# Optimization experiments

Hardware: AMD Instinct MI355X
Metric: run time of the kernel (lower is better)

## Reference

```python
import jax, jax.numpy as jnp
import numpy as np

T, D_IN, H, D_OUT = 20, 4, 768, 1
B = 1024


def setup_inputs() -> dict:
    key = jax.random.key(0)
    ks = jax.random.split(key, 8)
    s = 1.0 / np.sqrt(H)
    return {
        "batch_price": jax.random.normal(ks[0], (B, T, D_IN), jnp.float32),
        "batch_event": jax.random.normal(ks[1], (B, T, H), jnp.float32),
        "W_ih": jax.random.uniform(ks[2], (T, 4 * H, D_IN), jnp.float32, -s, s),
        "W_hh": jax.random.uniform(ks[3], (T, 4 * H, H), jnp.float32, -s, s),
        "b_ih": jax.random.uniform(ks[4], (T, 4 * H), jnp.float32, -s, s),
        "b_hh": jax.random.uniform(ks[5], (T, 4 * H), jnp.float32, -s, s),
        "fc_w": jax.random.uniform(ks[6], (D_OUT, H), jnp.float32, -s, s),
        "fc_b": jax.random.uniform(ks[7], (D_OUT,), jnp.float32, -s, s),
    }


def _lstm_cell(x, h_mat, c, wih, whh, bih, bhh):
    # gates: [B, 4H] in PyTorch LSTMCell order (i, f, g, o)
    gates = x @ wih.T + bih + h_mat @ whh.T + bhh
    i, f, g, o = jnp.split(gates, 4, axis=-1)
    c_next = jax.nn.sigmoid(f) * c + jax.nn.sigmoid(i) * jnp.tanh(g)
    h_next = jax.nn.sigmoid(o) * jnp.tanh(c_next)
    return h_next, c_next


def reference(batch_price, batch_event, W_ih, W_hh, b_ih, b_hh, fc_w, fc_b):
    Bb, Tt, _ = batch_price.shape
    Hh = W_hh.shape[-1]
    # step 0: hx = batch_event[:, 0], cell state = zeros
    h, c = _lstm_cell(batch_price[:, 0], batch_event[:, 0],
                      jnp.zeros((Bb, Hh), batch_price.dtype),
                      W_ih[0], W_hh[0], b_ih[0], b_hh[0])

    def step(carry, inp):
        h, c = carry
        x, ev, wih, whh, bih, bhh = inp
        # faithful to source: hx = torch.sum(batch_event_t + h_prev) -> scalar
        hx = jnp.sum(ev + h)
        h_mat = jnp.broadcast_to(hx, (Bb, Hh))
        h2, c2 = _lstm_cell(x, h_mat, c, wih, whh, bih, bhh)
        return (h2, c2), None

    xs = (jnp.swapaxes(batch_price[:, 1:], 0, 1),  # [T-1, B, D_IN]
          jnp.swapaxes(batch_event[:, 1:], 0, 1),  # [T-1, B, H]
          W_ih[1:], W_hh[1:], b_ih[1:], b_hh[1:])
    (h, c), _ = jax.lax.scan(step, (h, c), xs)
    return h @ fc_w.T + fc_b  # [B, 1]
```

## Files before the change

kernel.cpp:

```cpp
#include <hip/hip_runtime.h>
#include <stdint.h>

#define Bsz 1024
#define Tn  20
#define Hn  768
#define G4n 3072

#define WS_SH    0
#define WS_SEV   32
#define WS_PART  64
#define WS_RS    1088
#define WS_BS    (1088 + Tn*G4n)
#define WS_C     (1088 + 2*Tn*G4n)

#define NB_GEMM   768
#define NB_BIAS   240
#define NB_SEV    1216
#define NB_A      (NB_GEMM + NB_BIAS + NB_SEV)
#define NB_ROWSUM 3648

typedef float  floatx4 __attribute__((ext_vector_type(4)));
typedef short  bfrag8  __attribute__((ext_vector_type(8)));

__device__ __forceinline__ float wave_reduce(float v){
#pragma unroll
    for (int o = 32; o > 0; o >>= 1) v += __shfl_down(v, o, 64);
    return v;
}
__device__ __forceinline__ float sigf(float x){ return 1.0f/(1.0f+__expf(-x)); }
__device__ __forceinline__ float tanhfast(float x){ return 2.0f/(1.0f+__expf(-2.0f*x)) - 1.0f; }
__device__ __forceinline__ unsigned short f2bf_t(float f){
    return (unsigned short)(__float_as_uint(f) >> 16);
}
__device__ __forceinline__ float bf2f(unsigned short h){ return __uint_as_float(((uint32_t)h)<<16); }
__device__ __forceinline__ uint64_t pack_tv(unsigned t, float v){
    return ((uint64_t)t << 32) | (uint64_t)__float_as_uint(v);
}

__global__ void k_init(float* __restrict__ ws){
    for (int i = threadIdx.x; i < 1088; i += 1024) ws[i] = 0.0f;
}

__global__ __launch_bounds__(256) void k_gemm_sev(
    const float* __restrict__ price, const float* __restrict__ ev,
    const float* __restrict__ wih,   const float* __restrict__ whh,
    const float* __restrict__ bih,   const float* __restrict__ bhh,
    float* __restrict__ ws)
{
    __shared__ __align__(16) char smraw[4*64*56*2 + 16];
    unsigned short* Ah = (unsigned short*)smraw;
    unsigned short* Al = Ah + 64*56;
    unsigned short* Bh = Al + 64*56;
    unsigned short* Bl = Bh + 64*56;
    float* redk = (float*)(smraw + 4*64*56*2);
    float* red  = (float*)smraw;

    int blk = blockIdx.x, tid = threadIdx.x;

    if (blk < NB_GEMM) {
        float* Sh   = ws + WS_SH;
        float* cbuf = ws + WS_C;
        int bt = blk / 48, kt = blk % 48;
        int b0 = bt*64, k0 = kt*16;
        int w = tid >> 6, lane = tid & 63;
        int q = lane >> 4, col = lane & 15;

        int srow = tid >> 2;
        int kkoff = (tid & 3) * 8;
        int g_s = srow >> 4, rr = srow & 15;
        const float* aRow = ev  + (size_t)(b0 + srow)*(Tn*Hn);
        const float* bRow = whh + (size_t)(g_s*Hn + k0 + rr)*Hn;

        floatx4 acc[4];
#pragma unroll
        for (int g = 0; g < 4; ++g) acc[g] = (floatx4){0.f,0.f,0.f,0.f};

        for (int kk0 = 0; kk0 < Hn; kk0 += 32) {
            {
                const float* p = aRow + kk0 + kkoff;
                float4 v0 = *(const float4*)p;
                float4 v1 = *(const float4*)(p+4);
                float f[8] = {v0.x,v0.y,v0.z,v0.w,v1.x,v1.y,v1.z,v1.w};
                bfrag8 hv, lv;
#pragma unroll
                for (int i = 0; i < 8; ++i) {
                    unsigned short hb = f2bf_t(f[i]);
                    hv[i] = (short)hb;
                    lv[i] = (short)f2bf_t(f[i] - bf2f(hb));
                }
                *(bfrag8*)&Ah[srow*56 + kkoff] = hv;
                *(bfrag8*)&Al[srow*56 + kkoff] = lv;
                const float* pb = bRow + kk0 + kkoff;
                float4 u0 = *(const float4*)pb;
                float4 u1 = *(const float4*)(pb+4);
                float fb[8] = {u0.x,u0.y,u0.z,u0.w,u1.x,u1.y,u1.z,u1.w};
#pragma unroll
                for (int i = 0; i < 8; ++i) {
                    unsigned short hb = f2bf_t(fb[i]);
                    hv[i] = (short)hb;
                    lv[i] = (short)f2bf_t(fb[i] - bf2f(hb));
                }
                *(bfrag8*)&Bh[srow*56 + kkoff] = hv;
                *(bfrag8*)&Bl[srow*56 + kkoff] = lv;
            }
            __syncthreads();

            bfrag8 ah = *(const bfrag8*)&Ah[(w*16 + col)*56 + q*8];
            bfrag8 al = *(const bfrag8*)&Al[(w*16 + col)*56 + q*8];
#pragma unroll
            for (int g = 0; g < 4; ++g) {
                bfrag8 bh = *(const bfrag8*)&Bh[(g*16 + col)*56 + q*8];
                bfrag8 bl = *(const bfrag8*)&Bl[(g*16 + col)*56 + q*8];
                acc[g] = __builtin_amdgcn_mfma_f32_16x16x32_bf16(ah, bh, acc[g], 0,0,0);
                acc[g] = __builtin_amdgcn_mfma_f32_16x16x32_bf16(ah, bl, acc[g], 0,0,0);
                acc[g] = __builtin_amdgcn_mfma_f32_16x16x32_bf16(al, bh, acc[g], 0,0,0);
            }
            __syncthreads();
        }

        float hsum = 0.f;
#pragma unroll
        for (int r = 0; r < 4; ++r) {
            int b = b0 + w*16 + q*4 + r;
            float4 xv = *(const float4*)(price + (size_t)b*(Tn*4));
            float gates[4];
#pragma unroll
            for (int g = 0; g < 4; ++g) {
                int j = g*Hn + k0 + col;
                float4 wv = *(const float4*)(wih + (size_t)j*4);
                gates[g] = acc[g][r] + xv.x*wv.x + xv.y*wv.y + xv.z*wv.z + xv.w*wv.w
                         + bih[j] + bhh[j];
            }
            float c0 = sigf(gates[0]) * tanhfast(gates[2]);
            float h0 = sigf(gates[3]) * tanhfast(c0);
            cbuf[(size_t)b*Hn + k0 + col] = c0;
            hsum += h0;
        }
        hsum = wave_reduce(hsum);
        if (lane == 0) redk[w] = hsum;
        __syncthreads();
        if (tid == 0) atomicAdd(&ws[WS_SH], redk[0]+redk[1]+redk[2]+redk[3]);
        return;
    }

    blk -= NB_GEMM;
    float* Sev     = ws + WS_SEV;
    float* biassum = ws + WS_BS;

    if (blk < NB_BIAS) {
        int idx = blk*256 + tid;
        if (idx < Tn*G4n) biassum[idx] = bih[idx] + bhh[idx];
    } else {
        int sb = blk - NB_BIAS;
        int t  = 1 + (sb >> 6);
        int b0 = (sb & 63) * 16;
        float s = 0.f;
        for (int bb = 0; bb < 16; ++bb) {
            const float* base = ev + (size_t)(b0+bb)*(Tn*Hn) + (size_t)t*Hn;
            s += base[tid] + base[tid+256] + base[tid+512];
        }
        s = wave_reduce(s);
        if ((tid & 63) == 0) red[tid>>6] = s;
        __syncthreads();
        if (tid == 0) atomicAdd(&Sev[t], red[0]+red[1]+red[2]+red[3]);
    }
}

__global__ __launch_bounds__(256) void k_rowsum(
    const float* __restrict__ whh, float* __restrict__ ws)
{
    float* rowsum = ws + WS_RS;
    int tid = threadIdx.x, lane = tid & 63, wid = tid >> 6;
    int r0 = blockIdx.x*16 + wid*4;
    int t  = 1 + r0/G4n;
    int j0 = r0 - (t-1)*G4n;
    const float* base = whh + (size_t)t*G4n*Hn + (size_t)j0*Hn;

    float s[4];
#pragma unroll
    for (int rr = 0; rr < 4; ++rr) {
        const float* p = base + (size_t)rr*Hn + lane*4;
        float4 a = *(const float4*)p;
        float4 b = *(const float4*)(p + 256);
        float4 c = *(const float4*)(p + 512);
        s[rr] = (a.x+a.y)+(a.z+a.w) + (b.x+b.y)+(b.z+b.w) + (c.x+c.y)+(c.z+c.w);
    }
#pragma unroll
    for (int rr = 0; rr < 4; ++rr) s[rr] = wave_reduce(s[rr]);
    if (lane == 0) {
#pragma unroll
        for (int rr = 0; rr < 4; ++rr) rowsum[t*G4n + j0 + rr] = s[rr];
    }
}

__global__ __launch_bounds__(768) void k_steps(
    const float* __restrict__ price, const float* __restrict__ wih,
    const float* __restrict__ fcw,   const float* __restrict__ fcb,
    float* __restrict__ ws, float* __restrict__ out)
{
    __shared__ float pr[4][80];
    __shared__ float red[12];
    __shared__ float redP[4];
    __shared__ float redF[4][12];

    float* Sh  = ws + WS_SH;
    float* Sev = ws + WS_SEV;
    uint64_t* part = (uint64_t*)(ws + WS_PART);
    const float* rowsum  = ws + WS_RS;
    const float* biassum = ws + WS_BS;
    float* cbuf = ws + WS_C;

    int blk = blockIdx.x, tid = threadIdx.x;
    int lane = tid & 63, wid = tid >> 6;
    int k = tid;

    if (tid < 320) {
        int e = tid / 80, r = tid - e*80;
        pr[e][r] = price[(size_t)(blk + 256*e)*(Tn*4) + r];
    }

    float c[4];
#pragma unroll
    for (int e = 0; e < 4; ++e)
        c[e] = cbuf[(size_t)(blk + 256*e)*Hn + k];

    float fcwk = fcw[k];
    float fcb0 = fcb[0];
    __syncthreads();

    float hsum_prev = 0.f;
    float vout[4] = {0.f,0.f,0.f,0.f};

    for (int t = 1; t < Tn; ++t) {
        const float* wih_t = wih + (size_t)t*G4n*4;
        float rsv[4], base[4][4];
#pragma unroll
        for (int g = 0; g < 4; ++g) {
            int j = g*Hn + k;
            float4 wv = *(const float4*)(wih_t + (size_t)j*4);
            rsv[g]   = rowsum[t*G4n + j];
            float bs = biassum[t*G4n + j];
#pragma unroll
            for (int e = 0; e < 4; ++e) {
                base[e][g] = pr[e][t*4+0]*wv.x + pr[e][t*4+1]*wv.y
                           + pr[e][t*4+2]*wv.z + pr[e][t*4+3]*wv.w + bs;
            }
        }

        float hx;
        if (t == 1) {
            hx = Sev[1] + Sh[0];
        } else {
            int ph = (t-1) & 1;
            float v = wave_reduce(hsum_prev);
            if (lane == 0) red[wid] = v;
            __syncthreads();
            if (tid == 0) {
                float tot = 0.f;
#pragma unroll
                for (int i = 0; i < 12; ++i) tot += red[i];
                __hip_atomic_store(&part[ph*256 + blk], pack_tv((unsigned)(t-1), tot),
                                   __ATOMIC_RELAXED, __HIP_MEMORY_SCOPE_AGENT);
            }
            if (tid < 256) {
                uint64_t u;
                do { u = __hip_atomic_load(&part[ph*256 + tid], __ATOMIC_RELAXED, __HIP_MEMORY_SCOPE_AGENT); }
                while ((unsigned)(u >> 32) != (unsigned)(t-1));
                float pv = wave_reduce(__uint_as_float((uint32_t)u));
                if (lane == 0) redP[wid] = pv;
            }
            __syncthreads();
            hx = Sev[t] + ((redP[0]+redP[1]) + (redP[2]+redP[3]));
        }

        float hsum = 0.f;
#pragma unroll
        for (int e = 0; e < 4; ++e) {
            float gi = base[e][0] + hx*rsv[0];
            float gf = base[e][1] + hx*rsv[1];
            float gg = base[e][2] + hx*rsv[2];
            float go = base[e][3] + hx*rsv[3];
            float cn = sigf(gf)*c[e] + sigf(gi)*tanhfast(gg);
            c[e] = cn;
            float h = sigf(go)*tanhfast(cn);
            hsum += h;
            if (t == Tn-1) vout[e] = wave_reduce(h * fcwk);
        }
        hsum_prev = hsum;
    }

    if (lane == 0) {
#pragma unroll
        for (int e = 0; e < 4; ++e) redF[e][wid] = vout[e];
    }
    __syncthreads();
    if (tid < 4) {
        float tot = 0.f;
#pragma unroll
        for (int i = 0; i < 12; ++i) tot += redF[tid][i];
        out[blk + 256*tid] = tot + fcb0;
    }
}

extern "C" void kernel_launch(void* const* d_in, const int* in_sizes, int n_in,
                              void* d_out, int out_size, void* d_ws, size_t ws_size,
                              hipStream_t stream)
{
    const float* price = (const float*)d_in[0];
    const float* ev    = (const float*)d_in[1];
    const float* wih   = (const float*)d_in[2];
    const float* whh   = (const float*)d_in[3];
    const float* bih   = (const float*)d_in[4];
    const float* bhh   = (const float*)d_in[5];
    const float* fcw   = (const float*)d_in[6];
    const float* fcb   = (const float*)d_in[7];
    float* out = (float*)d_out;
    float* ws  = (float*)d_ws;

    k_init    <<<1, 1024, 0, stream>>>(ws);
    k_rowsum  <<<NB_ROWSUM, 256, 0, stream>>>(whh, ws);
    k_gemm_sev<<<NB_A, 256, 0, stream>>>(price, ev, wih, whh, bih, bhh, ws);
    k_steps   <<<256, 768, 0, stream>>>(price, wih, fcw, fcb, ws, out);
}
```

Measured before the change: 443.8 us.

## Use hierarchical two-level grid barrier for per-step hidden-sum reduction

Replaces the all-to-all per-step exchange, where every block polled all 256 partial sums, with a two-level tree. Each group of 32 blocks reports to a leader, the leaders exchange group sums and publish hx, and the other blocks poll a single word. It also folds the workspace zeroing into the rowsum kernel, which removes one kernel launch. This cuts global polling traffic, but the critical path per step now has more serial hops through the leaders.

New measurement: 441.6 us. Within noise of the previous version (-0.5%).

```diff
diff --git a/kernel.cpp b/kernel.cpp
--- a/kernel.cpp
+++ b/kernel.cpp
@@ -9,9 +9,10 @@
 #define WS_SH    0
 #define WS_SEV   32
 #define WS_PART  64
-#define WS_RS    1088
-#define WS_BS    (1088 + Tn*G4n)
-#define WS_C     (1088 + 2*Tn*G4n)
+#define WS_HXB   1120
+#define WS_RS    1152
+#define WS_BS    (1152 + Tn*G4n)
+#define WS_C     (1152 + 2*Tn*G4n)
 
 #define NB_GEMM   768
 #define NB_BIAS   240
@@ -35,10 +36,6 @@
 __device__ __forceinline__ float bf2f(unsigned short h){ return __uint_as_float(((uint32_t)h)<<16); }
 __device__ __forceinline__ uint64_t pack_tv(unsigned t, float v){
     return ((uint64_t)t << 32) | (uint64_t)__float_as_uint(v);
-}
-
-__global__ void k_init(float* __restrict__ ws){
-    for (int i = threadIdx.x; i < 1088; i += 1024) ws[i] = 0.0f;
 }
 
 __global__ __launch_bounds__(256) void k_gemm_sev(
@@ -58,7 +55,6 @@
     int blk = blockIdx.x, tid = threadIdx.x;
 
     if (blk < NB_GEMM) {
-        float* Sh   = ws + WS_SH;
         float* cbuf = ws + WS_C;
         int bt = blk / 48, kt = blk % 48;
         int b0 = bt*64, k0 = kt*16;
@@ -171,6 +167,9 @@
 {
     float* rowsum = ws + WS_RS;
     int tid = threadIdx.x, lane = tid & 63, wid = tid >> 6;
+    if (blockIdx.x == 0) {
+        for (int i = tid; i < WS_RS; i += 256) ws[i] = 0.0f;
+    }
     int r0 = blockIdx.x*16 + wid*4;
     int t  = 1 + r0/G4n;
     int j0 = r0 - (t-1)*G4n;
@@ -200,12 +199,13 @@
 {
     __shared__ float pr[4][80];
     __shared__ float red[12];
-    __shared__ float redP[4];
     __shared__ float redF[4][12];
+    __shared__ float shx;
 
     float* Sh  = ws + WS_SH;
     float* Sev = ws + WS_SEV;
     uint64_t* part = (uint64_t*)(ws + WS_PART);
+    uint64_t* hxb  = (uint64_t*)(ws + WS_HXB);
     const float* rowsum  = ws + WS_RS;
     const float* biassum = ws + WS_BS;
     float* cbuf = ws + WS_C;
@@ -213,6 +213,8 @@
     int blk = blockIdx.x, tid = threadIdx.x;
     int lane = tid & 63, wid = tid >> 6;
     int k = tid;
+    int g = blk >> 5, mi = blk & 31;
+    bool isLeader = (mi == 0);
 
     if (tid < 320) {
         int e = tid / 80, r = tid - e*80;
@@ -229,21 +231,20 @@
     __syncthreads();
 
     float hsum_prev = 0.f;
-    float vout[4] = {0.f,0.f,0.f,0.f};
 
     for (int t = 1; t < Tn; ++t) {
         const float* wih_t = wih + (size_t)t*G4n*4;
         float rsv[4], base[4][4];
 #pragma unroll
-        for (int g = 0; g < 4; ++g) {
-            int j = g*Hn + k;
+        for (int gg = 0; gg < 4; ++gg) {
+            int j = gg*Hn + k;
             float4 wv = *(const float4*)(wih_t + (size_t)j*4);
-            rsv[g]   = rowsum[t*G4n + j];
+            rsv[gg]  = rowsum[t*G4n + j];
             float bs = biassum[t*G4n + j];
 #pragma unroll
             for (int e = 0; e < 4; ++e) {
-                base[e][g] = pr[e][t*4+0]*wv.x + pr[e][t*4+1]*wv.y
-                           + pr[e][t*4+2]*wv.z + pr[e][t*4+3]*wv.w + bs;
+                base[e][gg] = pr[e][t*4+0]*wv.x + pr[e][t*4+1]*wv.y
+                            + pr[e][t*4+2]*wv.z + pr[e][t*4+3]*wv.w + bs;
             }
         }
 
@@ -252,25 +253,58 @@
             hx = Sev[1] + Sh[0];
         } else {
             int ph = (t-1) & 1;
+            unsigned tok = (unsigned)(t-1);
+            uint64_t* pp = part + (size_t)ph*264;
+
             float v = wave_reduce(hsum_prev);
             if (lane == 0) red[wid] = v;
             __syncthreads();
+            float tot = 0.f;
             if (tid == 0) {
-                float tot = 0.f;
 #pragma unroll
                 for (int i = 0; i < 12; ++i) tot += red[i];
-                __hip_atomic_store(&part[ph*256 + blk], pack_tv((unsigned)(t-1), tot),
-                                   __ATOMIC_RELAXED, __HIP_MEMORY_SCOPE_AGENT);
-            }
-            if (tid < 256) {
-                uint64_t u;
-                do { u = __hip_atomic_load(&part[ph*256 + tid], __ATOMIC_RELAXED, __HIP_MEMORY_SCOPE_AGENT); }
-                while ((unsigned)(u >> 32) != (unsigned)(t-1));
-                float pv = wave_reduce(__uint_as_float((uint32_t)u));
-                if (lane == 0) redP[wid] = pv;
+                if (!isLeader)
+                    __hip_atomic_store(&pp[g*32 + mi], pack_tv(tok, tot),
+                                       __ATOMIC_RELAXED, __HIP_MEMORY_SCOPE_AGENT);
+            }
+            if (isLeader) {
+                if (tid < 64) {
+                    float pv = 0.f;
+                    if (tid >= 1 && tid < 32) {
+                        uint64_t u;
+                        do { u = __hip_atomic_load(&pp[g*32 + tid], __ATOMIC_RELAXED, __HIP_MEMORY_SCOPE_AGENT); }
+                        while ((unsigned)(u >> 32) != tok);
+                        pv = __uint_as_float((uint32_t)u);
+                    } else if (tid == 0) pv = tot;
+                    float gsum = wave_reduce(pv);
+                    if (tid == 0)
+                        __hip_atomic_store(&pp[256 + g], pack_tv(tok, gsum),
+                                           __ATOMIC_RELAXED, __HIP_MEMORY_SCOPE_AGENT);
+                    float gv = 0.f;
+                    if (tid < 8) {
+                        uint64_t u;
+                        do { u = __hip_atomic_load(&pp[256 + tid], __ATOMIC_RELAXED, __HIP_MEMORY_SCOPE_AGENT); }
+                        while ((unsigned)(u >> 32) != tok);
+                        gv = __uint_as_float((uint32_t)u);
+                    }
+                    float tota = wave_reduce(gv);
+                    if (tid == 0) {
+                        float hxv = Sev[t] + tota;
+                        shx = hxv;
+                        __hip_atomic_store(&hxb[ph*8 + g], pack_tv((unsigned)t, hxv),
+                                           __ATOMIC_RELAXED, __HIP_MEMORY_SCOPE_AGENT);
+                    }
+                }
+            } else {
+                if (tid == 0) {
+                    uint64_t u;
+                    do { u = __hip_atomic_load(&hxb[ph*8 + g], __ATOMIC_RELAXED, __HIP_MEMORY_SCOPE_AGENT); }
+                    while ((unsigned)(u >> 32) != (unsigned)t);
+                    shx = __uint_as_float((uint32_t)u);
+                }
             }
             __syncthreads();
-            hx = Sev[t] + ((redP[0]+redP[1]) + (redP[2]+redP[3]));
+            hx = shx;
         }
 
         float hsum = 0.f;
@@ -278,21 +312,20 @@
         for (int e = 0; e < 4; ++e) {
             float gi = base[e][0] + hx*rsv[0];
             float gf = base[e][1] + hx*rsv[1];
-            float gg = base[e][2] + hx*rsv[2];
+            float gg2 = base[e][2] + hx*rsv[2];
             float go = base[e][3] + hx*rsv[3];
-            float cn = sigf(gf)*c[e] + sigf(gi)*tanhfast(gg);
+            float cn = sigf(gf)*c[e] + sigf(gi)*tanhfast(gg2);
             c[e] = cn;
             float h = sigf(go)*tanhfast(cn);
             hsum += h;
-            if (t == Tn-1) vout[e] = wave_reduce(h * fcwk);
+            if (t == Tn-1) {
+                float vo = wave_reduce(h * fcwk);
+                if (lane == 0) redF[e][wid] = vo;
+            }
         }
         hsum_prev = hsum;
     }
 
-    if (lane == 0) {
-#pragma unroll
-        for (int e = 0; e < 4; ++e) redF[e][wid] = vout[e];
-    }
     __syncthreads();
     if (tid < 4) {
         float tot = 0.f;
@@ -317,7 +350,6 @@
     float* out = (float*)d_out;
     float* ws  = (float*)d_ws;
 
-    k_init    <<<1, 1024, 0, stream>>>(ws);
     k_rowsum  <<<NB_ROWSUM, 256, 0, stream>>>(whh, ws);
     k_gemm_sev<<<NB_A, 256, 0, stream>>>(price, ev, wih, whh, bih, bhh, ws);
     k_steps   <<<256, 768, 0, stream>>>(price, wih, fcw, fcb, ws, out);
```
